# Kernel tuning notes

Measured on AMD Instinct MI355X. Metric: run time of the kernel, lower is better.

Reference implementation:

```python
import jax, jax.numpy as jnp
import numpy as np

B, T, C, H = 4, 2048, 1024, 16
HD = C // H  # head dim = 64


def _rope(x, pos):
    """Rotary embedding. x: [B,H,T,hd], pos: [B,T] int positions."""
    half = x.shape[-1] // 2
    inv_freq = 1.0 / (10000.0 ** (jnp.arange(half, dtype=jnp.float32) / half))
    ang = pos.astype(jnp.float32)[:, None, :, None] * inv_freq  # [B,1,T,half]
    cos, sin = jnp.cos(ang), jnp.sin(ang)
    x1, x2 = x[..., :half], x[..., half:]
    return jnp.concatenate([x1 * cos - x2 * sin, x1 * sin + x2 * cos], axis=-1)


def setup_inputs() -> dict:
    key = jax.random.key(0)
    k1, k2, k3 = jax.random.split(key, 3)
    x = jax.random.normal(k1, (B, T, C), dtype=jnp.float32)
    W_attn = jax.random.normal(k2, (C, 3 * C), dtype=jnp.float32) * (1.0 / np.sqrt(C))
    W_proj = jax.random.normal(k3, (C, C), dtype=jnp.float32) * (1.0 / np.sqrt(C))
    indices = jnp.broadcast_to(jnp.arange(T, dtype=jnp.int32)[None, :], (B, T))
    return {"x": x, "W_attn": W_attn, "W_proj": W_proj, "indices": indices}


def reference(x, W_attn, W_proj, indices):
    # QKV projection (bias=False)
    qkv = x @ W_attn  # [B,T,3C]
    q, k, v = jnp.split(qkv, 3, axis=-1)

    def to_heads(t):
        return t.reshape(B, T, H, HD).transpose(0, 2, 1, 3)  # [B,H,T,hd]

    q, k, v = to_heads(q), to_heads(k), to_heads(v)
    # RoPE on q and k at positions given by indices (pos_emb_closure.adapt_*)
    q = _rope(q, indices)
    k = _rope(k, indices)

    # attn_mask = k_indices <= q_indices, shape [B,1,T,T]
    mask = indices[:, None, None, :] <= indices[:, None, :, None]

    att = jnp.einsum("bhqd,bhkd->bhqk", q, k) * (1.0 / np.sqrt(HD))
    att = jnp.where(mask, att, jnp.float32(-jnp.inf))
    att = jax.nn.softmax(att, axis=-1)
    y = jnp.einsum("bhqk,bhkd->bhqd", att, v)  # [B,H,T,hd]
    y = y.transpose(0, 2, 1, 3).reshape(B, T, C)
    return y @ W_proj
```

## Files before the change

kernel.cpp:

```cpp
#include <hip/hip_runtime.h>
#include <math.h>

namespace {
constexpr int Bsz = 4;
constexpr int T   = 2048;
constexpr int C   = 1024;
constexpr int H   = 16;
constexpr int HD  = 64;

typedef short bf16x8 __attribute__((ext_vector_type(8)));
typedef float f32x4  __attribute__((ext_vector_type(4)));

#if defined(__has_builtin)
#if __has_builtin(__builtin_amdgcn_global_load_lds)
#define HAVE_GLL 1
typedef __attribute__((address_space(3))) unsigned int lds_u32_t;
typedef __attribute__((address_space(1))) unsigned int g_u32_t;
#define GLL16(gp, lp)                                                        \
  __builtin_amdgcn_global_load_lds((const g_u32_t*)(gp), (lds_u32_t*)(lp),   \
                                   16, 0, 0)
#endif
#endif

__device__ __forceinline__ unsigned short f2bf(float f) {
  unsigned int u = __builtin_bit_cast(unsigned int, f);
  u += 0x7FFFu + ((u >> 16) & 1u);
  return (unsigned short)(u >> 16);
}
__device__ __forceinline__ float bf2f(unsigned short s) {
  unsigned int u = ((unsigned int)s) << 16;
  return __builtin_bit_cast(float, u);
}
__device__ __forceinline__ unsigned int cvtpk_bf16(float a, float b) {
  unsigned int r;
  asm("v_cvt_pk_bf16_f32 %0, %1, %2" : "=v"(r) : "v"(a), "v"(b));
  return r;
}

__global__ __launch_bounds__(256) void f32_to_bf16_kernel(
    const float* __restrict__ in, unsigned short* __restrict__ out, int n4) {
  int i = blockIdx.x * 256 + threadIdx.x;
  if (i < n4) {
    float4 v = ((const float4*)in)[i];
    ushort4 o;
    o.x = f2bf(v.x); o.y = f2bf(v.y); o.z = f2bf(v.z); o.w = f2bf(v.w);
    ((ushort4*)out)[i] = o;
  }
}

__global__ __launch_bounds__(256) void transpose_bf16_kernel(
    const float* __restrict__ W, unsigned short* __restrict__ Wt, int K, int N) {
  __shared__ float tile[32][33];
  const int n0 = blockIdx.x * 32, k0 = blockIdx.y * 32;
  const int r = threadIdx.x >> 3, c4 = threadIdx.x & 7;
  float4 v = *(const float4*)(W + (size_t)(k0 + r) * N + n0 + c4 * 4);
  tile[r][c4 * 4 + 0] = v.x;
  tile[r][c4 * 4 + 1] = v.y;
  tile[r][c4 * 4 + 2] = v.z;
  tile[r][c4 * 4 + 3] = v.w;
  __syncthreads();
  ushort4 o;
  o.x = f2bf(tile[c4 * 4 + 0][r]);
  o.y = f2bf(tile[c4 * 4 + 1][r]);
  o.z = f2bf(tile[c4 * 4 + 2][r]);
  o.w = f2bf(tile[c4 * 4 + 3][r]);
  *(ushort4*)(Wt + (size_t)(n0 + r) * K + k0 + c4 * 4) = o;
}

template <int MODE>
__global__ __launch_bounds__(256) void gemm_bt(
    const unsigned short* __restrict__ A, const unsigned short* __restrict__ Bt,
    float* __restrict__ Cout, unsigned short* __restrict__ qp,
    unsigned short* __restrict__ kp, unsigned short* __restrict__ vp,
    int M, int N, int K) {
  __shared__ __align__(16) unsigned short As[128 * 32];
  __shared__ __align__(16) unsigned short Bs[128 * 32];
  const int tid = threadIdx.x;
  const int lane = tid & 63, w = tid >> 6;
  const int wr = w & 1, wc = w >> 1;
  const int l15 = lane & 15, quad = lane >> 4;
  const int m0 = blockIdx.y * 128, n0 = blockIdx.x * 128;

  const int srow = lane >> 2;
  const int schunk = (lane & 3) * 8;
  const unsigned short* gA = A + (size_t)(m0 + w * 32 + srow) * K + schunk;
  const unsigned short* gB = Bt + (size_t)(n0 + w * 32 + srow) * K + schunk;
  unsigned short* lA0 = &As[(w * 32) * 32 + lane * 8];
  unsigned short* lA1 = &As[(w * 32 + 16) * 32 + lane * 8];
  unsigned short* lB0 = &Bs[(w * 32) * 32 + lane * 8];
  unsigned short* lB1 = &Bs[(w * 32 + 16) * 32 + lane * 8];

  f32x4 acc[4][4] = {};

  for (int k0 = 0; k0 < K; k0 += 32) {
    __syncthreads();
#ifdef HAVE_GLL
    GLL16(gA + k0, lA0);
    GLL16(gA + (size_t)16 * K + k0, lA1);
    GLL16(gB + k0, lB0);
    GLL16(gB + (size_t)16 * K + k0, lB1);
#else
    *(uint4*)lA0 = *(const uint4*)(gA + k0);
    *(uint4*)lA1 = *(const uint4*)(gA + (size_t)16 * K + k0);
    *(uint4*)lB0 = *(const uint4*)(gB + k0);
    *(uint4*)lB1 = *(const uint4*)(gB + (size_t)16 * K + k0);
#endif
    __syncthreads();

    bf16x8 af[4], bfr[4];
#pragma unroll
    for (int mf = 0; mf < 4; ++mf)
      af[mf] = *(const bf16x8*)&As[(wr * 64 + mf * 16 + l15) * 32 + quad * 8];
#pragma unroll
    for (int nf = 0; nf < 4; ++nf)
      bfr[nf] = *(const bf16x8*)&Bs[(wc * 64 + nf * 16 + l15) * 32 + quad * 8];
#pragma unroll
    for (int mf = 0; mf < 4; ++mf)
#pragma unroll
      for (int nf = 0; nf < 4; ++nf)
        acc[mf][nf] = __builtin_amdgcn_mfma_f32_16x16x32_bf16(
            af[mf], bfr[nf], acc[mf][nf], 0, 0, 0);
  }

#pragma unroll
  for (int mf = 0; mf < 4; ++mf) {
    const int row0 = m0 + wr * 64 + mf * 16 + quad * 4;
#pragma unroll
    for (int nf = 0; nf < 4; ++nf) {
      if (MODE == 0) {
#pragma unroll
        for (int r = 0; r < 4; ++r) {
          const int col = n0 + wc * 64 + nf * 16 + l15;
          Cout[(size_t)(row0 + r) * N + col] = acc[mf][nf][r];
        }
      } else {
        const int col = n0 + wc * 64 + nf * 16 + l15;
        const int which = col >> 10;
        const int rem = col & (C - 1);
        const int h = rem >> 6, hd = rem & 63;
        const int b = row0 >> 11, t0 = row0 & (T - 1);
        if (which == 2) {
          ushort4 pv;
          pv.x = f2bf(acc[mf][nf][0]);
          pv.y = f2bf(acc[mf][nf][1]);
          pv.z = f2bf(acc[mf][nf][2]);
          pv.w = f2bf(acc[mf][nf][3]);
          *(ushort4*)(vp + (((size_t)(b * H + h)) * HD + hd) * T + t0) = pv;
        } else {
          unsigned short* dst = which == 0 ? qp : kp;
#pragma unroll
          for (int r = 0; r < 4; ++r)
            dst[(((size_t)(b * H + h)) * T + t0 + r) * HD + hd] =
                f2bf(acc[mf][nf][r]);
        }
      }
    }
  }
}

__global__ __launch_bounds__(256) void rope_bf16(unsigned short* __restrict__ q,
                                                 unsigned short* __restrict__ k,
                                                 const int* __restrict__ idx) {
  const int g = blockIdx.x * 8 + (threadIdx.x >> 5);
  const int lane = threadIdx.x & 31;
  const int b = g >> 11, t = g & (T - 1);
  const int pos = idx[b * T + t];
  const float inv = exp2f((float)lane * -0.41524101186f);
  float sn, cs;
  sincosf((float)pos * inv, &sn, &cs);
  const float SC = 0.18033688f;
  const float snq = sn * SC, csq = cs * SC;
  const size_t base0 = ((size_t)b * H * T + t) * HD + lane;
#pragma unroll 4
  for (int h = 0; h < H; ++h) {
    const size_t base = base0 + (size_t)h * T * HD;
    float x1 = bf2f(q[base]), x2 = bf2f(q[base + 32]);
    q[base]      = f2bf(x1 * csq - x2 * snq);
    q[base + 32] = f2bf(x1 * snq + x2 * csq);
    x1 = bf2f(k[base]);
    x2 = bf2f(k[base + 32]);
    k[base]      = f2bf(x1 * cs - x2 * sn);
    k[base + 32] = f2bf(x1 * sn + x2 * cs);
  }
}

__global__ __launch_bounds__(256) void flash_attn_mfma(
    const unsigned short* __restrict__ q, const unsigned short* __restrict__ k,
    const unsigned short* __restrict__ vt, const int* __restrict__ idx,
    unsigned short* __restrict__ y) {
  __shared__ __align__(16) unsigned short Ks[2][64 * 64];
  __shared__ __align__(16) unsigned short Vts[2][64 * 64];
  __shared__ __align__(16) unsigned short Pq[64 * 64];

  const int tid = threadIdx.x;
  const int lane = tid & 63, w = tid >> 6;
  const int l15 = lane & 15, quad = lane >> 4;

  const int flat = (blockIdx.z * H + blockIdx.y) * 16 + blockIdx.x;
  const int slot = flat >> 3;
  const int bh_i = (flat & 7) * 8 + (slot >> 4);
  const int bx = slot & 15;
  const int h = bh_i & (H - 1), b = bh_i >> 4;

  const size_t bh = (size_t)bh_i;
  const unsigned short* qg = q + bh * T * HD;
  const unsigned short* kg = k + bh * T * HD;
  const unsigned short* vg = vt + bh * HD * T;
  const int* idxb = idx + b * T;

  int km;
  {
    const int4* p4 = (const int4*)(idxb + (lane << 5));
    int4 v0 = p4[0];
    int m = max(max(v0.x, v0.y), max(v0.z, v0.w));
#pragma unroll
    for (int j = 1; j < 8; ++j) {
      int4 v = p4[j];
      m = max(m, max(max(v.x, v.y), max(v.z, v.w)));
    }
    km = max(m, __shfl_xor(m, 1));
  }

  const int r1 = tid >> 3, c1 = tid & 7;
  const int r2 = r1 + 32;
  const int swS1 = r1 * 64 + ((c1 * 8) ^ ((r1 & 7) << 3));
  const int swS2 = r2 * 64 + ((c1 * 8) ^ ((r1 & 7) << 3));
  const int rx = (l15 & 7) << 3;

  for (int ti = 0; ti < 2; ++ti) {
    const int qt = (ti == 0) ? bx : 31 - bx;
    const int q0 = qt * 64;
    const int qrow = q0 + w * 16 + l15;

    const bf16x8 bq0 = *(const bf16x8*)(qg + (size_t)qrow * HD + quad * 8);
    const bf16x8 bq1 = *(const bf16x8*)(qg + (size_t)qrow * HD + 32 + quad * 8);
    const int pq = idxb[qrow];
    int mq = pq;
    mq = min(mq, __shfl_xor(mq, 1));
    mq = min(mq, __shfl_xor(mq, 2));
    mq = min(mq, __shfl_xor(mq, 4));
    mq = min(mq, __shfl_xor(mq, 8));

    float m_run = -1e38f, l_run = 0.0f;
    f32x4 Oa[4] = {};

    {
      uint4 ka = *(const uint4*)(kg + (size_t)r1 * HD + c1 * 8);
      uint4 kb = *(const uint4*)(kg + (size_t)r2 * HD + c1 * 8);
      uint4 va = *(const uint4*)(vg + (size_t)r1 * T + c1 * 8);
      uint4 vb = *(const uint4*)(vg + (size_t)r2 * T + c1 * 8);
      __syncthreads();
      *(uint4*)&Ks[0][swS1] = ka;
      *(uint4*)&Ks[0][swS2] = kb;
      *(uint4*)&Vts[0][swS1] = va;
      *(uint4*)&Vts[0][swS2] = vb;
    }

    for (int kt = 0; kt <= qt; ++kt) {
      const int cur = kt & 1;
      const int k0 = kt * 64;
      __syncthreads();

      uint4 nka, nkb, nva, nvb;
      if (kt < qt) {
        const int kn = k0 + 64;
        nka = *(const uint4*)(kg + (size_t)(kn + r1) * HD + c1 * 8);
        nkb = *(const uint4*)(kg + (size_t)(kn + r2) * HD + c1 * 8);
        nva = *(const uint4*)(vg + (size_t)r1 * T + kn + c1 * 8);
        nvb = *(const uint4*)(vg + (size_t)r2 * T + kn + c1 * 8);
      }

      f32x4 Sa[4];
      __builtin_amdgcn_s_setprio(1);
#pragma unroll
      for (int nf = 0; nf < 4; ++nf) {
        const int row = (nf * 16 + l15) * 64;
        bf16x8 ak0 = *(const bf16x8*)&Ks[cur][row + ((quad * 8) ^ rx)];
        bf16x8 ak1 = *(const bf16x8*)&Ks[cur][row + ((32 + quad * 8) ^ rx)];
        f32x4 s = {};
        s = __builtin_amdgcn_mfma_f32_16x16x32_bf16(ak0, bq0, s, 0, 0, 0);
        s = __builtin_amdgcn_mfma_f32_16x16x32_bf16(ak1, bq1, s, 0, 0, 0);
        Sa[nf] = s;
      }
      __builtin_amdgcn_s_setprio(0);

      const int kmt = __shfl(km, kt << 1);
      if (kmt > mq) {
#pragma unroll
        for (int nf = 0; nf < 4; ++nf) {
          const int4 pk4 = *(const int4*)(idxb + k0 + nf * 16 + quad * 4);
          if (pk4.x > pq) Sa[nf][0] = -3e38f;
          if (pk4.y > pq) Sa[nf][1] = -3e38f;
          if (pk4.z > pq) Sa[nf][2] = -3e38f;
          if (pk4.w > pq) Sa[nf][3] = -3e38f;
        }
      }

      float mx = fmaxf(
          fmaxf(fmaxf(fmaxf(Sa[0][0], Sa[0][1]), Sa[0][2]),
                fmaxf(fmaxf(Sa[0][3], Sa[1][0]), Sa[1][1])),
          fmaxf(fmaxf(fmaxf(Sa[1][2], Sa[1][3]), Sa[2][0]),
                fmaxf(fmaxf(Sa[2][1], Sa[2][2]), Sa[2][3])));
      mx = fmaxf(mx, fmaxf(fmaxf(Sa[3][0], Sa[3][1]), fmaxf(Sa[3][2], Sa[3][3])));
      mx = fmaxf(mx, __shfl_xor(mx, 16));
      mx = fmaxf(mx, __shfl_xor(mx, 32));

      if (!__all(mx <= m_run + 8.0f)) {
        const float mn = fmaxf(m_run, mx);
        const float alpha = exp2f(m_run - mn);
        m_run = mn;
        l_run *= alpha;
#pragma unroll
        for (int nfd = 0; nfd < 4; ++nfd)
#pragma unroll
          for (int r = 0; r < 4; ++r) Oa[nfd][r] *= alpha;
      }

      float s0 = 0.f, s1 = 0.f, s2 = 0.f, s3 = 0.f;
#pragma unroll
      for (int nf = 0; nf < 4; ++nf) {
        float p0 = exp2f(Sa[nf][0] - m_run);
        float p1 = exp2f(Sa[nf][1] - m_run);
        float p2 = exp2f(Sa[nf][2] - m_run);
        float p3 = exp2f(Sa[nf][3] - m_run);
        Sa[nf][0] = p0; Sa[nf][1] = p1; Sa[nf][2] = p2; Sa[nf][3] = p3;
        s0 += p0; s1 += p1; s2 += p2; s3 += p3;
      }
      float sum = (s0 + s1) + (s2 + s3);
      sum += __shfl_xor(sum, 16);
      sum += __shfl_xor(sum, 32);
      l_run += sum;

      {
        const int prow = (w * 16 + l15) * 64;
#pragma unroll
        for (int nf = 0; nf < 4; ++nf) {
          uint2 pw;
          pw.x = cvtpk_bf16(Sa[nf][0], Sa[nf][1]);
          pw.y = cvtpk_bf16(Sa[nf][2], Sa[nf][3]);
          *(uint2*)&Pq[prow + ((nf * 16 + quad * 4) ^ rx)] = pw;
        }
      }

      asm volatile("s_waitcnt lgkmcnt(0)" ::: "memory");

      const int prow = (w * 16 + l15) * 64;
      const bf16x8 bp0 = *(const bf16x8*)&Pq[prow + ((quad * 8) ^ rx)];
      const bf16x8 bp1 = *(const bf16x8*)&Pq[prow + ((32 + quad * 8) ^ rx)];

      __builtin_amdgcn_s_setprio(1);
#pragma unroll
      for (int nfd = 0; nfd < 4; ++nfd) {
        const int vrow = (nfd * 16 + l15) * 64;
        bf16x8 av0 = *(const bf16x8*)&Vts[cur][vrow + ((quad * 8) ^ rx)];
        bf16x8 av1 = *(const bf16x8*)&Vts[cur][vrow + ((32 + quad * 8) ^ rx)];
        Oa[nfd] = __builtin_amdgcn_mfma_f32_16x16x32_bf16(av0, bp0, Oa[nfd], 0, 0, 0);
        Oa[nfd] = __builtin_amdgcn_mfma_f32_16x16x32_bf16(av1, bp1, Oa[nfd], 0, 0, 0);
      }
      __builtin_amdgcn_s_setprio(0);

      if (kt < qt) {
        const int nxt = cur ^ 1;
        *(uint4*)&Ks[nxt][swS1] = nka;
        *(uint4*)&Ks[nxt][swS2] = nkb;
        *(uint4*)&Vts[nxt][swS1] = nva;
        *(uint4*)&Vts[nxt][swS2] = nvb;
      }
    }

    const float rl = 1.0f / l_run;
    const size_t base = ((size_t)b * T + qrow) * (size_t)C + h * HD;
#pragma unroll
    for (int nfd = 0; nfd < 4; ++nfd) {
      ushort4 o;
      o.x = f2bf(Oa[nfd][0] * rl);
      o.y = f2bf(Oa[nfd][1] * rl);
      o.z = f2bf(Oa[nfd][2] * rl);
      o.w = f2bf(Oa[nfd][3] * rl);
      *(ushort4*)(y + base + nfd * 16 + quad * 4) = o;
    }
  }
}

}

extern "C" void kernel_launch(void* const* d_in, const int* in_sizes, int n_in,
                              void* d_out, int out_size, void* d_ws,
                              size_t ws_size, hipStream_t stream) {
  const float* x      = (const float*)d_in[0];
  const float* W_attn = (const float*)d_in[1];
  const float* W_proj = (const float*)d_in[2];
  const int* indices  = (const int*)d_in[3];
  float* out = (float*)d_out;

  const size_t nM = (size_t)Bsz * T * C;
  unsigned short* xb  = (unsigned short*)d_ws;
  unsigned short* wat = xb + nM;
  unsigned short* wpt = wat + (size_t)3 * C * C;
  unsigned short* qp  = wpt + (size_t)C * C;
  unsigned short* kp  = qp + nM;
  unsigned short* vp  = kp + nM;
  unsigned short* yb  = vp + nM;

  f32_to_bf16_kernel<<<(int)(nM / 4 / 256), 256, 0, stream>>>(x, xb, (int)(nM / 4));
  transpose_bf16_kernel<<<dim3(3 * C / 32, C / 32), 256, 0, stream>>>(W_attn, wat, C, 3 * C);
  transpose_bf16_kernel<<<dim3(C / 32, C / 32), 256, 0, stream>>>(W_proj, wpt, C, C);
  gemm_bt<1><<<dim3(3 * C / 128, Bsz * T / 128), 256, 0, stream>>>(
      xb, wat, nullptr, qp, kp, vp, Bsz * T, 3 * C, C);
  rope_bf16<<<(Bsz * T) / 8, 256, 0, stream>>>(qp, kp, indices);
  flash_attn_mfma<<<dim3(16, H, Bsz), 256, 0, stream>>>(qp, kp, vp, indices, yb);
  gemm_bt<0><<<dim3(C / 128, Bsz * T / 128), 256, 0, stream>>>(
      yb, wpt, out, nullptr, nullptr, nullptr, Bsz * T, C, C);
}
```

Baseline: 313.0 us.

## Keep softmax P in registers by permuting V^T LDS layout to match MFMA operand

The Pq shared-memory round trip for the probability tile is removed: P is packed straight from the S accumulator registers into the B operand of the PV MFMA. To make that valid, V^T rows are stored into LDS with a permuted column order so the k-dimension matches the register layout of P. The row-sum is now kept per lane and reduced across lanes once at the end instead of every tile, and the per-tile mask check reads a precomputed ballot instead of a shuffle. This saves LDS writes, reads and a waitcnt per tile, but splits V stores into smaller 8-byte writes.

```diff
diff --git a/kernel.cpp b/kernel.cpp
--- a/kernel.cpp
+++ b/kernel.cpp
@@ -10,6 +10,7 @@
 
 typedef short bf16x8 __attribute__((ext_vector_type(8)));
 typedef float f32x4  __attribute__((ext_vector_type(4)));
+typedef unsigned int u32x4 __attribute__((ext_vector_type(4)));
 
 #if defined(__has_builtin)
 #if __has_builtin(__builtin_amdgcn_global_load_lds)
@@ -190,16 +191,15 @@
     unsigned short* __restrict__ y) {
   __shared__ __align__(16) unsigned short Ks[2][64 * 64];
   __shared__ __align__(16) unsigned short Vts[2][64 * 64];
-  __shared__ __align__(16) unsigned short Pq[64 * 64];
 
   const int tid = threadIdx.x;
   const int lane = tid & 63, w = tid >> 6;
   const int l15 = lane & 15, quad = lane >> 4;
 
   const int flat = (blockIdx.z * H + blockIdx.y) * 16 + blockIdx.x;
-  const int slot = flat >> 3;
-  const int bh_i = (flat & 7) * 8 + (slot >> 4);
-  const int bx = slot & 15;
+  const int slot_ = flat >> 3;
+  const int bh_i = (flat & 7) * 8 + (slot_ >> 4);
+  const int bx = slot_ & 15;
   const int h = bh_i & (H - 1), b = bh_i >> 4;
 
   const size_t bh = (size_t)bh_i;
@@ -223,14 +223,19 @@
 
   const int r1 = tid >> 3, c1 = tid & 7;
   const int r2 = r1 + 32;
-  const int swS1 = r1 * 64 + ((c1 * 8) ^ ((r1 & 7) << 3));
-  const int swS2 = r2 * 64 + ((c1 * 8) ^ ((r1 & 7) << 3));
+  const int xr1 = (r1 & 7) << 3;
+  const int swS1 = r1 * 64 + ((c1 * 8) ^ xr1);
+  const int swS2 = r2 * 64 + ((c1 * 8) ^ xr1);
+  const int vbase = 32 * (c1 >> 2) + 16 * (c1 & 1) + 4 * ((c1 >> 1) & 1);
+  const int vo1a = r1 * 64 + ((vbase + 0) ^ xr1);
+  const int vo1b = r1 * 64 + ((vbase + 8) ^ xr1);
+  const int vo2a = r2 * 64 + ((vbase + 0) ^ xr1);
+  const int vo2b = r2 * 64 + ((vbase + 8) ^ xr1);
   const int rx = (l15 & 7) << 3;
 
   for (int ti = 0; ti < 2; ++ti) {
     const int qt = (ti == 0) ? bx : 31 - bx;
-    const int q0 = qt * 64;
-    const int qrow = q0 + w * 16 + l15;
+    const int qrow = qt * 64 + w * 16 + l15;
 
     const bf16x8 bq0 = *(const bf16x8*)(qg + (size_t)qrow * HD + quad * 8);
     const bf16x8 bq1 = *(const bf16x8*)(qg + (size_t)qrow * HD + 32 + quad * 8);
@@ -240,8 +245,9 @@
     mq = min(mq, __shfl_xor(mq, 2));
     mq = min(mq, __shfl_xor(mq, 4));
     mq = min(mq, __shfl_xor(mq, 8));
-
-    float m_run = -1e38f, l_run = 0.0f;
+    const unsigned long long bal = __ballot(km > mq);
+
+    float m_run = -1e38f, lq = 0.0f;
     f32x4 Oa[4] = {};
 
     {
@@ -252,8 +258,10 @@
       __syncthreads();
       *(uint4*)&Ks[0][swS1] = ka;
       *(uint4*)&Ks[0][swS2] = kb;
-      *(uint4*)&Vts[0][swS1] = va;
-      *(uint4*)&Vts[0][swS2] = vb;
+      *(uint2*)&Vts[0][vo1a] = make_uint2(va.x, va.y);
+      *(uint2*)&Vts[0][vo1b] = make_uint2(va.z, va.w);
+      *(uint2*)&Vts[0][vo2a] = make_uint2(vb.x, vb.y);
+      *(uint2*)&Vts[0][vo2b] = make_uint2(vb.z, vb.w);
     }
 
     for (int kt = 0; kt <= qt; ++kt) {
@@ -284,8 +292,7 @@
       }
       __builtin_amdgcn_s_setprio(0);
 
-      const int kmt = __shfl(km, kt << 1);
-      if (kmt > mq) {
+      if ((bal >> (kt + kt)) & 1ull) {
 #pragma unroll
         for (int nf = 0; nf < 4; ++nf) {
           const int4 pk4 = *(const int4*)(idxb + k0 + nf * 16 + quad * 4);
@@ -309,14 +316,14 @@
         const float mn = fmaxf(m_run, mx);
         const float alpha = exp2f(m_run - mn);
         m_run = mn;
-        l_run *= alpha;
+        lq *= alpha;
 #pragma unroll
         for (int nfd = 0; nfd < 4; ++nfd)
 #pragma unroll
           for (int r = 0; r < 4; ++r) Oa[nfd][r] *= alpha;
       }
 
-      float s0 = 0.f, s1 = 0.f, s2 = 0.f, s3 = 0.f;
+      u32x4 w0, w1;
 #pragma unroll
       for (int nf = 0; nf < 4; ++nf) {
         float p0 = exp2f(Sa[nf][0] - m_run);
@@ -324,29 +331,16 @@
         float p2 = exp2f(Sa[nf][2] - m_run);
         float p3 = exp2f(Sa[nf][3] - m_run);
         Sa[nf][0] = p0; Sa[nf][1] = p1; Sa[nf][2] = p2; Sa[nf][3] = p3;
-        s0 += p0; s1 += p1; s2 += p2; s3 += p3;
-      }
-      float sum = (s0 + s1) + (s2 + s3);
-      sum += __shfl_xor(sum, 16);
-      sum += __shfl_xor(sum, 32);
-      l_run += sum;
-
-      {
-        const int prow = (w * 16 + l15) * 64;
-#pragma unroll
-        for (int nf = 0; nf < 4; ++nf) {
-          uint2 pw;
-          pw.x = cvtpk_bf16(Sa[nf][0], Sa[nf][1]);
-          pw.y = cvtpk_bf16(Sa[nf][2], Sa[nf][3]);
-          *(uint2*)&Pq[prow + ((nf * 16 + quad * 4) ^ rx)] = pw;
+        if (nf < 2) {
+          w0[nf * 2 + 0] = cvtpk_bf16(p0, p1);
+          w0[nf * 2 + 1] = cvtpk_bf16(p2, p3);
+        } else {
+          w1[(nf - 2) * 2 + 0] = cvtpk_bf16(p0, p1);
+          w1[(nf - 2) * 2 + 1] = cvtpk_bf16(p2, p3);
         }
       }
-
-      asm volatile("s_waitcnt lgkmcnt(0)" ::: "memory");
-
-      const int prow = (w * 16 + l15) * 64;
-      const bf16x8 bp0 = *(const bf16x8*)&Pq[prow + ((quad * 8) ^ rx)];
-      const bf16x8 bp1 = *(const bf16x8*)&Pq[prow + ((32 + quad * 8) ^ rx)];
+      const bf16x8 bp0 = __builtin_bit_cast(bf16x8, w0);
+      const bf16x8 bp1 = __builtin_bit_cast(bf16x8, w1);
 
       __builtin_amdgcn_s_setprio(1);
 #pragma unroll
@@ -359,16 +353,26 @@
       }
       __builtin_amdgcn_s_setprio(0);
 
+      lq += ((Sa[0][0] + Sa[0][1]) + (Sa[0][2] + Sa[0][3])) +
+            ((Sa[1][0] + Sa[1][1]) + (Sa[1][2] + Sa[1][3])) +
+            ((Sa[2][0] + Sa[2][1]) + (Sa[2][2] + Sa[2][3])) +
+            ((Sa[3][0] + Sa[3][1]) + (Sa[3][2] + Sa[3][3]));
+
       if (kt < qt) {
         const int nxt = cur ^ 1;
         *(uint4*)&Ks[nxt][swS1] = nka;
         *(uint4*)&Ks[nxt][swS2] = nkb;
-        *(uint4*)&Vts[nxt][swS1] = nva;
-        *(uint4*)&Vts[nxt][swS2] = nvb;
+        *(uint2*)&Vts[nxt][vo1a] = make_uint2(nva.x, nva.y);
+        *(uint2*)&Vts[nxt][vo1b] = make_uint2(nva.z, nva.w);
+        *(uint2*)&Vts[nxt][vo2a] = make_uint2(nvb.x, nvb.y);
+        *(uint2*)&Vts[nxt][vo2b] = make_uint2(nvb.z, nvb.w);
       }
     }
 
-    const float rl = 1.0f / l_run;
+    float lsum = lq;
+    lsum += __shfl_xor(lsum, 16);
+    lsum += __shfl_xor(lsum, 32);
+    const float rl = 1.0f / lsum;
     const size_t base = ((size_t)b * T + qrow) * (size_t)C + h * HD;
 #pragma unroll
     for (int nfd = 0; nfd < 4; ++nfd) {
```

Result: faster. 304.5 us (-2.7%).
